# Optimization experiments

Hardware: AMD Instinct MI355X
Metric: run time of the kernel (lower is better)

The kernel has to match this reference:

```python
import jax, jax.numpy as jnp
import numpy as np

B = 1024      # jets per batch
P = 150       # TOTAL_PARTICLES per jet
N = B * P     # total nodes
DEG = 16      # avg degree
E = N * DEG
H = 256       # GNN_HIDDEN_DIM
K = 6         # GNN_K
NC = 10       # NUM_CLUSTERS
IN = 3


def setup_inputs() -> dict:
    key = jax.random.key(0)
    ks = jax.random.split(key, 16)
    x = jax.random.normal(ks[0], (N, IN), jnp.float32)
    # kNN-like within-jet edges: each node sends to DEG random nodes of its own jet
    src = jnp.repeat(jnp.arange(N, dtype=jnp.int32), DEG)
    tgt = (src // P) * P + jax.random.randint(ks[1], (E,), 0, P, dtype=jnp.int32)
    edge_index = jnp.stack([src, tgt])  # [2, E]
    batch = jnp.arange(N, dtype=jnp.int32) // P  # sorted graph ids, exactly P per graph
    inp = dict(x=x, edge_index=edge_index, batch=batch)
    dims = [(IN, H), (H, H), (H, H), (H, H)]
    for i, (di, do) in enumerate(dims):
        s = 1.0 / np.sqrt(di)
        inp[f"W{i+1}"] = jax.random.uniform(ks[2 + i], (K, di, do), jnp.float32, -s, s)
        inp[f"b{i+1}"] = jnp.zeros((do,), jnp.float32)
    for i in range(3):
        inp[f"g{i+1}"] = jnp.ones((H,), jnp.float32)
        inp[f"be{i+1}"] = jnp.zeros((H,), jnp.float32)
    inp["centers"] = jax.random.normal(ks[10], (NC, 2), jnp.float32) * 0.2
    inp["log_temp"] = jnp.float32(2.0)
    return inp


def _lap_weights(src, tgt, n):
    # PyG ChebConv norm with lambda_max=2, sym normalization, self-loops removed:
    # scaled Laplacian L_hat = -D^{-1/2} A D^{-1/2} (zero diagonal)
    w = (src != tgt).astype(jnp.float32)          # remove self-loops
    deg = jax.ops.segment_sum(w, src, num_segments=n)
    dis = jnp.where(deg > 0, 1.0 / jnp.sqrt(deg), 0.0)
    return -(dis[src] * w * dis[tgt])             # [E]


def _cheb(x, W, b, src, tgt, lw, n):
    # Chebyshev recurrence: T0=x, T1=Lx, Tk=2L T_{k-1} - T_{k-2}
    prop = lambda h: jax.ops.segment_sum(lw[:, None] * h[src], tgt, num_segments=n)
    Tx0 = x
    out = Tx0 @ W[0]
    Tx1 = prop(Tx0)
    out = out + Tx1 @ W[1]
    for k in range(2, W.shape[0]):
        Tx2 = 2.0 * prop(Tx1) - Tx0
        out = out + Tx2 @ W[k]
        Tx0, Tx1 = Tx1, Tx2
    return out + b


def _bn(h, g, b):
    # BatchNorm1d, training-mode batch statistics (biased var), eps=1e-5
    m = h.mean(0)
    v = h.var(0)
    return (h - m) * jax.lax.rsqrt(v + 1e-5) * g + b


def reference(x, edge_index, batch, W1, b1, W2, b2, W3, b3, W4, b4,
              g1, be1, g2, be2, g3, be3, centers, log_temp):
    n = x.shape[0]
    src, tgt = edge_index[0], edge_index[1]
    lw = _lap_weights(src, tgt, n)
    lrelu = lambda h: jax.nn.leaky_relu(h, 0.01)
    h = lrelu(_bn(_cheb(x, W1, b1, src, tgt, lw, n), g1, be1))
    h = lrelu(_bn(_cheb(h, W2, b2, src, tgt, lw, n), g2, be2))
    h = lrelu(_bn(_cheb(h, W3, b3, src, tgt, lw, n), g3, be3))
    h = _cheb(h, W4, b4, src, tgt, lw, n)
    h = h / jnp.maximum(jnp.linalg.norm(h, axis=1, keepdims=True), 1e-12)  # F.normalize
    # to_dense_batch: batch is sorted with exactly P nodes per graph -> pure reshape,
    # node_mask is all True
    dense_h = h.reshape(B, P, -1)          # [B, P, H]
    dense_c = x[:, :2].reshape(B, P, 2)    # (eta, phi)
    dist = ((dense_c[:, :, None, :] - centers) ** 2).sum(-1)   # [B, P, NC]
    T = jnp.exp(jnp.clip(log_temp, -2.0, 3.0))
    assignment = jax.nn.softmax(-T * dist, axis=-1)            # mask is all-true
    pooled = jnp.einsum('bnk,bnd->bkd', assignment, dense_h)   # [B, NC, H]
    pooled = pooled / (assignment.sum(1)[:, :, None] + 1e-8)
    return pooled.reshape(B, -1)  # [B, NC*H]
```

## Files before the change

### kernel.cpp

```cpp
#include <hip/hip_runtime.h>
#include <cstdio>

#define NODES 153600
#define PJ 150
#define NJETS 1024
#define DEG 16
#define NEDGE (NODES*DEG)
#define HD 256
#define NCL 10

#define LSTR 192
#define TNS  64

typedef unsigned short u16;
typedef _Float16 f16;
typedef f16 f16x8 __attribute__((ext_vector_type(8)));
typedef u16 u16x8 __attribute__((ext_vector_type(8)));
typedef u16 u16x4 __attribute__((ext_vector_type(4)));
typedef float f32x4 __attribute__((ext_vector_type(4)));

__device__ inline float h2f(u16 u) { union { u16 s; f16 h; } v; v.s = u; return (float)v.h; }
__device__ inline u16 f2h(float f) { union { u16 s; f16 h; } v; v.h = (f16)f; return v.s; }
__device__ inline int swz(int seg, int key) { return (seg & ~7) | ((seg & 7) ^ (key & 7)); }

__global__ void k_diag(float* out, float code) {
  if (blockIdx.x == 0 && threadIdx.x == 0) out[0] = code;
}


__global__ __launch_bounds__(256) void k_discounts(const int* __restrict__ tgt,
                                                   int* __restrict__ counts,
                                                   float* __restrict__ dis) {
  int i = blockIdx.x*256 + threadIdx.x;
  if (i < NEDGE) atomicAdd(&counts[tgt[i]], 1);
  if (i < NODES) {
    int cnt = 0;
#pragma unroll
    for (int j = 0; j < DEG; ++j) cnt += (tgt[i*DEG + j] != i) ? 1 : 0;
    dis[i] = (cnt > 0) ? rsqrtf((float)cnt) : 0.f;
  }
}

__global__ __launch_bounds__(256) void k_scan(const int* __restrict__ counts, int* __restrict__ rowptr, int* __restrict__ cursor) {
  int j = blockIdx.x*256 + threadIdx.x;
  if (j >= NJETS) return;
  int run = j*PJ*DEG;
  for (int l = 0; l < PJ; ++l) {
    int idx = j*PJ + l;
    int cnt = counts[idx];
    rowptr[idx] = run;
    cursor[idx] = run;
    run += cnt;
  }
  if (j == 0) rowptr[NODES] = NEDGE;
}

__global__ __launch_bounds__(256) void k_fill(const int* __restrict__ src_, const int* __restrict__ tgt_,
                                              const float* __restrict__ dis, int* __restrict__ cursor,
                                              unsigned char* __restrict__ ccol, float* __restrict__ cw) {
  int e = blockIdx.x*256 + threadIdx.x;
  if (e >= NEDGE) return;
  int s = src_[e], t = tgt_[e];
  int pos = atomicAdd(&cursor[t], 1);
  ccol[pos] = (unsigned char)(s % PJ);
  cw[pos] = (s != t) ? -(dis[s]*dis[t]) : 0.f;
}

__global__ __launch_bounds__(256) void k_prepLW(const int* __restrict__ rowptr,
                                                const unsigned char* __restrict__ ccol,
                                                const float* __restrict__ cw,
                                                u16* __restrict__ Lg,
                                                const float* __restrict__ Wa, const float* __restrict__ Wb,
                                                const float* __restrict__ Wc, u16* __restrict__ WT,
                                                float* __restrict__ s1, float* __restrict__ s2,
                                                float* __restrict__ rn) {
  int bid = blockIdx.x, tid = threadIdx.x;
  if (bid < NJETS) {
    int j = bid;
    u16* L = Lg + (size_t)j*160*160;
    if (tid < 160) {
      u16x8 z = {0,0,0,0,0,0,0,0};
      for (int seg = 0; seg < 20; ++seg) *(u16x8*)&L[tid*160 + seg*8] = z;
      if (tid < PJ) {
        int es = rowptr[j*PJ + tid], ee = rowptr[j*PJ + tid + 1];
        u16* row = L + tid*160;
        for (int e = es; e < ee; ++e) {
          int c = (int)ccol[e];
          row[c] = f2h(h2f(row[c]) + 2.f*cw[e]);
        }
      }
    }
  } else {
    int i = (bid - NJETS)*256 + tid;
    if (i < 3*256*1536) {
      int layer = i / (256*1536);
      int rem = i - layer*(256*1536);
      int cout = rem / 1536, k = rem - cout*1536;
      int term = k >> 8, cin = k & 255;
      const float* W = (layer == 0) ? Wa : (layer == 1) ? Wb : Wc;
      WT[i] = f2h(W[(size_t)term*65536 + cin*256 + cout]);
    }
    if (i < 2*HD) { s1[i] = 0.f; s2[i] = 0.f; }
    if (i < NODES) rn[i] = 0.f;
  }
}

__global__ __launch_bounds__(512) void k_cheb3(const float* __restrict__ x,
                                               const int* __restrict__ rowptr,
                                               const unsigned char* __restrict__ ccol,
                                               const float* __restrict__ cw,
                                               float* __restrict__ tall,
                                               float* __restrict__ s0) {
  __shared__ float Ta[450], Tb[450];
  __shared__ float cw_s[PJ*DEG];
  __shared__ u16  col_s[PJ*DEG];
  __shared__ int  rp_s[PJ+1];
  int j = blockIdx.x, tid = threadIdx.x;
  if (j == 0 && tid < 2*HD) s0[tid] = 0.f;
  int jb = j*PJ, e0 = jb*DEG;
  for (int i = tid; i < PJ*DEG; i += 512) { cw_s[i] = cw[e0+i]; col_s[i] = (u16)ccol[e0+i]; }
  for (int i = tid; i < PJ+1; i += 512) rp_s[i] = rowptr[jb+i] - e0;
  if (tid < 450) Ta[tid] = x[(size_t)jb*3 + tid];
  __syncthreads();
  int r = tid/3, c = tid - r*3;
  float* cur = Ta; float* oth = Tb;
  if (tid < 450) tall[(size_t)(jb+r)*18 + c] = cur[tid];
  for (int t = 1; t < 6; ++t) {
    if (tid < 450) {
      int es = rp_s[r], ee = rp_s[r+1];
      float acc = 0.f;
      for (int e = es; e < ee; ++e) acc += cw_s[e]*cur[(int)col_s[e]*3 + c];
      float v = (t == 1) ? acc : 2.f*acc - oth[tid];
      oth[tid] = v;
      tall[(size_t)(jb+r)*18 + t*3 + c] = v;
    }
    __syncthreads();
    float* tmp = cur; cur = oth; oth = tmp;
  }
}

__global__ __launch_bounds__(256) void k_gemm1(const float* __restrict__ tall, const float* __restrict__ W1,
                                               const float* __restrict__ b1, float* __restrict__ stats,
                                               u16* __restrict__ outc) {
  __shared__ float wl[18*256];
  __shared__ float tl[64*18];
  int c = threadIdx.x;
  for (int i = c; i < 18*256; i += 256) wl[i] = W1[i];
  int n0 = blockIdx.x*64;
  __syncthreads();
  for (int i = c; i < 64*18; i += 256) tl[i] = tall[(size_t)n0*18 + i];
  __syncthreads();
  float bc = b1[c];
  float s = 0.f, s2 = 0.f;
  for (int n = 0; n < 64; ++n) {
    float acc = 0.f;
#pragma unroll
    for (int i = 0; i < 18; ++i) acc += tl[n*18 + i] * wl[i*256 + c];
    outc[(size_t)(n0+n)*HD + c] = f2h(acc);
    float vb = acc + bc;
    s += vb; s2 += vb*vb;
  }
  atomicAdd(&stats[c], s);
  atomicAdd(&stats[HD + c], s2);
}

template<int OMODE>
__global__ __launch_bounds__(1024, 4) void k_cheb(const u16* __restrict__ IN,
                                                  const u16* __restrict__ WTu,
                                                  const u16* __restrict__ Lg,
                                                  const float* __restrict__ statsPrev,
                                                  const float* __restrict__ gP,
                                                  const float* __restrict__ beP,
                                                  const float* __restrict__ bP,
                                                  const float* __restrict__ bCur,
                                                  float* __restrict__ statsCur,
                                                  float* __restrict__ rn,
                                                  u16* __restrict__ OUTp) {
  __shared__ u16 Ls[160*LSTR];
  __shared__ u16 Tn[2][160*TNS];
  __shared__ u16 Tt[2][64*LSTR];
  __shared__ float bnA[HD], bnB[HD];
  int j = blockIdx.x, tid = threadIdx.x;
  int jb = j*PJ;
  int lane = tid & 63, wid = tid >> 6;
  int wm = wid >> 3, wn = wid & 7;
  int lr = lane & 15, lg = lane >> 4;
  int ph = wn >> 2, cs = wn & 3;
  int cown = cs*16 + lr;
  int key   = lr & 7;
  int segA0 = ((lg    ) ^ key) * 8;
  int segA1 = ((lg + 4) ^ key) * 8;
  int pOff[5] = { segA0, segA1, 64 + segA0, 64 + segA1, 128 + segA0 };
  int ep0 = ((cown >> 3) ^ ((lg & 1)*4 + 0)) * 8 + (cown & 7);
  int ep1 = ((cown >> 3) ^ ((lg & 1)*4 + 1)) * 8 + (cown & 7);
  int ep2 = ((cown >> 3) ^ ((lg & 1)*4 + 2)) * 8 + (cown & 7);
  int ep3 = ((cown >> 3) ^ ((lg & 1)*4 + 3)) * 8 + (cown & 7);
  int cownL = cown * LSTR;
  const f16* WT = (const f16*)WTu;
  const f16* wtb = WT + (size_t)(wn*32 + lr)*1536 + lg*8;

  if (tid < HD) {
    const float invN = 1.f/(float)NODES;
    float m = statsPrev[tid]*invN;
    float var = statsPrev[HD+tid]*invN - m*m;
    float A = rsqrtf(var + 1e-5f) * gP[tid];
    bnA[tid] = A;
    bnB[tid] = (bP[tid] - m)*A + beP[tid];
  }
  {
    const u16* src = Lg + (size_t)j*25600;
    for (int i = tid; i < 3200; i += 1024) {
      int row = i/20, seg = i - row*20;
      *(u16x8*)&Ls[row*LSTR + swz(seg,row)*8] = *(const u16x8*)&src[row*160 + seg*8];
    }
  }
  f32x4 acc[5][2];
#pragma unroll
  for (int a = 0; a < 5; ++a)
#pragma unroll
    for (int b = 0; b < 2; ++b) acc[a][b] = (f32x4)0.f;

  u16x4 tc0, tc1, tc2, tc3, tc4, tp0, tp1, tp2, tp3, tp4;

  for (int qp = 0; qp < 2; ++qp) {
    __syncthreads();
    for (int i = tid; i < 2560; i += 1024) {
      int h = (i >= 1280) ? 1 : 0;
      int rem = i - h*1280;
      int row = rem >> 3, seg = rem & 7;
      u16x8 o = {0,0,0,0,0,0,0,0};
      if (row < PJ) {
        int c0 = (qp*2+h)*64 + seg*8;
        u16x8 v = *(const u16x8*)&IN[(size_t)(jb+row)*HD + c0];
#pragma unroll
        for (int u = 0; u < 8; ++u) {
          float f = h2f(v[u])*bnA[c0+u] + bnB[c0+u];
          o[u] = f2h((f > 0.f) ? f : 0.01f*f);
        }
      }
      *(u16x8*)&Tn[h][row*TNS + (seg ^ (row & 7))*8] = o;
    }
    __syncthreads();
    for (int i = tid; i < 2560; i += 1024) {
      int h = (i >= 1280) ? 1 : 0;
      int rem = i - h*1280;
      int c = rem & 63, m = rem >> 6;
      u16x8 v;
#pragma unroll
      for (int u = 0; u < 8; ++u) {
        int r = m*8 + u;
        v[u] = Tn[h][r*TNS + ((c >> 3) ^ (r & 7))*8 + (c & 7)];
      }
      *(u16x8*)&Tt[h][c*LSTR + swz(m, c)*8] = v;
    }
#define TINIT(MF, TC, TP) { int r0 = wm*80 + MF*16 + lg*4; u16x4 t; \
    t[0] = Tn[ph][(r0+0)*TNS + ep0]; t[1] = Tn[ph][(r0+1)*TNS + ep1]; \
    t[2] = Tn[ph][(r0+2)*TNS + ep2]; t[3] = Tn[ph][(r0+3)*TNS + ep3]; \
    TC = t; TP = t; }
    TINIT(0, tc0, tp0) TINIT(1, tc1, tp1) TINIT(2, tc2, tp2) TINIT(3, tc3, tp3) TINIT(4, tc4, tp4)
#undef TINIT
    __syncthreads();
#pragma unroll 1
    for (int t = 0; t < 6; ++t) {
#pragma unroll
      for (int h = 0; h < 2; ++h) {
        int kbase = t*256 + (qp*2+h)*64;
#pragma unroll
        for (int ks = 0; ks < 64; ks += 32) {
          int segA = (ks == 0) ? segA0 : segA1;
          f16x8 a[5], bv[2];
#pragma unroll
          for (int nf = 0; nf < 2; ++nf)
            bv[nf] = *(const f16x8*)&wtb[nf*24576 + kbase + ks];
#pragma unroll
          for (int mf = 0; mf < 5; ++mf) {
            int row = wm*80 + mf*16 + lr;
            a[mf] = *(const f16x8*)&Tn[h][row*TNS + segA];
          }
#pragma unroll
          for (int nf = 0; nf < 2; ++nf)
#pragma unroll
            for (int mf = 0; mf < 5; ++mf)
              acc[mf][nf] = __builtin_amdgcn_mfma_f32_16x16x32_f16(a[mf], bv[nf], acc[mf][nf], 0, 0, 0);
        }
      }
      if (t < 5) {
        f32x4 pacc[5];
#pragma unroll
        for (int mf = 0; mf < 5; ++mf) pacc[mf] = (f32x4)0.f;
#pragma unroll
        for (int ks = 0; ks < 5; ++ks) {
          f16x8 b = *(const f16x8*)&Tt[ph][cownL + pOff[ks]];
#pragma unroll
          for (int mf = 0; mf < 5; ++mf) {
            int row = wm*80 + mf*16 + lr;
            f16x8 a = *(const f16x8*)&Ls[row*LSTR + pOff[ks]];
            pacc[mf] = __builtin_amdgcn_mfma_f32_16x16x32_f16(a, b, pacc[mf], 0, 0, 0);
          }
        }
        __syncthreads();
#define TEPI(MF, TC, TP) { int r0 = wm*80 + MF*16 + lg*4; u16x4 o; \
        { float v0_ = (t == 0) ? 0.5f*pacc[MF][0] : pacc[MF][0] - h2f(TP[0]); o[0] = f2h(v0_); } \
        { float v1_ = (t == 0) ? 0.5f*pacc[MF][1] : pacc[MF][1] - h2f(TP[1]); o[1] = f2h(v1_); } \
        { float v2_ = (t == 0) ? 0.5f*pacc[MF][2] : pacc[MF][2] - h2f(TP[2]); o[2] = f2h(v2_); } \
        { float v3_ = (t == 0) ? 0.5f*pacc[MF][3] : pacc[MF][3] - h2f(TP[3]); o[3] = f2h(v3_); } \
        Tn[ph][(r0+0)*TNS + ep0] = o[0]; Tn[ph][(r0+1)*TNS + ep1] = o[1]; \
        Tn[ph][(r0+2)*TNS + ep2] = o[2]; Tn[ph][(r0+3)*TNS + ep3] = o[3]; \
        int sgT = wm*10 + MF*2 + (lg >> 1); \
        int segT = (sgT & ~7) | ((sgT & 7) ^ key); \
        *(u16x4*)&Tt[ph][cownL + segT*8 + (lg & 1)*4] = o; \
        TP = TC; TC = o; }
        TEPI(0, tc0, tp0) TEPI(1, tc1, tp1) TEPI(2, tc2, tp2) TEPI(3, tc3, tp3) TEPI(4, tc4, tp4)
#undef TEPI
        __syncthreads();
      }
    }
  }
  if (OMODE == 0) {
#pragma unroll
    for (int nf = 0; nf < 2; ++nf) {
      int col = wn*32 + nf*16 + lr;
      float bc = bCur[col];
      float s = 0.f, s2 = 0.f;
#pragma unroll
      for (int mf = 0; mf < 5; ++mf) {
        int row = wm*80 + mf*16 + lg*4;
#pragma unroll
        for (int e = 0; e < 4; ++e) {
          int r = row + e;
          if (r < PJ) {
            float v = acc[mf][nf][e];
            OUTp[(size_t)(jb+r)*HD + col] = f2h(v);
            float vb = v + bc;
            s += vb; s2 += vb*vb;
          }
        }
      }
      s  += __shfl_xor(s, 16, 64);  s  += __shfl_xor(s, 32, 64);
      s2 += __shfl_xor(s2, 16, 64); s2 += __shfl_xor(s2, 32, 64);
      if (lg == 0) {
        atomicAdd(&statsCur[col], s);
        atomicAdd(&statsCur[HD + col], s2);
      }
    }
  } else {
    float bc[2];
#pragma unroll
    for (int nf = 0; nf < 2; ++nf) bc[nf] = bCur[wn*32 + nf*16 + lr];
#pragma unroll
    for (int mf = 0; mf < 5; ++mf) {
      int row = wm*80 + mf*16 + lg*4;
#pragma unroll
      for (int e = 0; e < 4; ++e) {
        int r = row + e;
        float srow = 0.f;
        if (r < PJ) {
#pragma unroll
          for (int nf = 0; nf < 2; ++nf) {
            int col = wn*32 + nf*16 + lr;
            float v = acc[mf][nf][e];
            OUTp[(size_t)(jb+r)*HD + col] = f2h(v);
            float vb = v + bc[nf];
            srow += vb*vb;
          }
        }
        srow += __shfl_xor(srow, 1, 64);
        srow += __shfl_xor(srow, 2, 64);
        srow += __shfl_xor(srow, 4, 64);
        srow += __shfl_xor(srow, 8, 64);
        if (lr == 0 && r < PJ) atomicAdd(&rn[jb + r], srow);
      }
    }
  }
}


__global__ __launch_bounds__(256) void k_pool(const u16* __restrict__ h, const float* __restrict__ rn,
                                              const float* __restrict__ bias, const float* __restrict__ x,
                                              const float* __restrict__ centers, const float* __restrict__ log_temp,
                                              float* __restrict__ out) {
  __shared__ float a_s[PJ][NCL];
  __shared__ float colsum[NCL];
  __shared__ float inv_s[PJ];
  int j = blockIdx.x;
  int tid = threadIdx.x;
  float T = expf(fminf(fmaxf(log_temp[0], -2.f), 3.f));
  if (tid < PJ) {
    int g = j*PJ + tid;
    inv_s[tid] = 1.f / fmaxf(sqrtf(rn[g]), 1e-12f);
    float eta = x[(size_t)g*3], phi = x[(size_t)g*3 + 1];
    float d[NCL];
    float dmin = 1e30f;
#pragma unroll
    for (int k = 0; k < NCL; ++k) {
      float dx = eta - centers[2*k], dy = phi - centers[2*k+1];
      d[k] = dx*dx + dy*dy;
      dmin = fminf(dmin, d[k]);
    }
    float s = 0.f, ek[NCL];
#pragma unroll
    for (int k = 0; k < NCL; ++k) { ek[k] = expf(-T*(d[k]-dmin)); s += ek[k]; }
    float invs = 1.f/s;
#pragma unroll
    for (int k = 0; k < NCL; ++k) a_s[tid][k] = ek[k]*invs;
  }
  __syncthreads();
  if (tid < NCL) {
    float s = 0.f;
    for (int n = 0; n < PJ; ++n) s += a_s[n][tid];
    colsum[tid] = s;
  }
  __syncthreads();
  int c = tid;
  float bc = bias[c];
  float acc[NCL] = {};
  for (int n = 0; n < PJ; ++n) {
    float hv = (h2f(h[(size_t)(j*PJ + n)*HD + c]) + bc) * inv_s[n];
#pragma unroll
    for (int k = 0; k < NCL; ++k) acc[k] += a_s[n][k]*hv;
  }
#pragma unroll
  for (int k = 0; k < NCL; ++k)
    out[(size_t)j*(NCL*HD) + k*HD + c] = acc[k] / (colsum[k] + 1e-8f);
}


extern "C" void kernel_launch(void* const* d_in, const int* in_sizes, int n_in,
                              void* d_out, int out_size, void* d_ws, size_t ws_size,
                              hipStream_t stream) {
  (void)in_sizes; (void)n_in; (void)out_size;
  const float* x   = (const float*)d_in[0];
  const int*   ei  = (const int*)d_in[1];
  const int*   srcA = ei;
  const int*   tgtA = ei + NEDGE;
  const float* W1  = (const float*)d_in[3];
  const float* b1  = (const float*)d_in[4];
  const float* W2  = (const float*)d_in[5];
  const float* b2  = (const float*)d_in[6];
  const float* W3  = (const float*)d_in[7];
  const float* b3  = (const float*)d_in[8];
  const float* W4  = (const float*)d_in[9];
  const float* b4  = (const float*)d_in[10];
  const float* g1  = (const float*)d_in[11];
  const float* be1 = (const float*)d_in[12];
  const float* g2  = (const float*)d_in[13];
  const float* be2 = (const float*)d_in[14];
  const float* g3  = (const float*)d_in[15];
  const float* be3 = (const float*)d_in[16];
  const float* centers  = (const float*)d_in[17];
  const float* log_temp = (const float*)d_in[18];
  float* out = (float*)d_out;

  auto rb = [](size_t b) { return (b + 255) & ~(size_t)255; };
  size_t need = 3*rb((size_t)NODES*HD*2)
              + 3*rb((size_t)NODES*4)
              + rb((size_t)(NODES+1)*4)
              + rb((size_t)NEDGE)
              + rb((size_t)NEDGE*4)
              + rb((size_t)3*2*HD*4)
              + rb((size_t)NODES*4);
  fprintf(stderr, "[kernel_launch] ws_size=%zu need=%zu\n", ws_size, need);
  if (d_ws == nullptr || ws_size < need) {
    float code = 1.0e6f + (float)(ws_size >> 20);
    k_diag<<<1, 1, 0, stream>>>(out, code);
    return;
  }

  char* wp = (char*)d_ws;
  auto alloc = [&](size_t b) -> void* {
    void* p = (void*)wp;
    wp += (b + 255) & ~(size_t)255;
    return p;
  };
  u16*   OUTA = (u16*)alloc((size_t)NODES*HD*2);
  u16*   OUTB = (u16*)alloc((size_t)NODES*HD*2);
  u16*   Y    = (u16*)alloc((size_t)NODES*HD*2);
  float* dis  = (float*)alloc((size_t)NODES*4);
  int*   counts = (int*)alloc((size_t)NODES*4);
  int*   cursor = (int*)alloc((size_t)NODES*4);
  int*   rowptr = (int*)alloc((size_t)(NODES+1)*4);
  unsigned char* ccol = (unsigned char*)alloc((size_t)NEDGE);
  float* cw     = (float*)alloc((size_t)NEDGE*4);
  float* stats  = (float*)alloc((size_t)3*2*HD*4);
  float* rn     = (float*)alloc((size_t)NODES*4);
  float* Tall = (float*)Y;
  u16*   Lg   = Y;
  u16*   Wcat = Y + (size_t)NJETS*160*160;
  float* s0 = stats, *s1 = stats + 512, *s2 = stats + 1024;

  hipMemsetAsync(counts, 0, (size_t)NODES*4, stream);
  k_discounts<<<(NEDGE+255)/256, 256, 0, stream>>>(tgtA, counts, dis);
  k_scan<<<(NJETS+255)/256, 256, 0, stream>>>(counts, rowptr, cursor);
  k_fill<<<(NEDGE+255)/256, 256, 0, stream>>>(srcA, tgtA, dis, cursor, ccol, cw);

  k_cheb3<<<NJETS, 512, 0, stream>>>(x, rowptr, ccol, cw, Tall, s0);
  k_gemm1<<<NODES/64, 256, 0, stream>>>(Tall, W1, b1, s0, OUTA);

  k_prepLW<<<NJETS + (3*256*1536+255)/256, 256, 0, stream>>>(rowptr, ccol, cw, Lg,
                                                             W2, W3, W4, Wcat, s1, s2, rn);

  k_cheb<0><<<NJETS, 1024, 0, stream>>>(OUTA, Wcat,            Lg, s0, g1, be1, b1, b2, s1, rn, OUTB);
  k_cheb<0><<<NJETS, 1024, 0, stream>>>(OUTB, Wcat + 393216,   Lg, s1, g2, be2, b2, b3, s2, rn, OUTA);
  k_cheb<1><<<NJETS, 1024, 0, stream>>>(OUTA, Wcat + 2*393216, Lg, s2, g3, be3, b3, b4, s2, rn, OUTB);

  k_pool<<<NJETS, 256, 0, stream>>>(OUTB, rn, b4, x, centers, log_temp, out);
}
```

Baseline: 1.351 ms.

## Fuse layer-1 Chebyshev with its GEMM and build dense Laplacian in-kernel

Merges k_cheb3 and k_gemm1 into one per-jet kernel so the Chebyshev terms stay in shared memory and are never written to and re-read from global memory. The dense per-jet Laplacian is no longer materialised in global memory by k_prepLW; each k_cheb block zeroes its shared tile and scatters the CSR edges into it directly. The edge scatter is repeated in each of the three layer kernels and runs serially per row inside the block, and padding rows are zeroed once instead of on every load. This removes about 50MB of global Laplacian traffic and one launch, and shrinks the workspace.

```diff
diff --git a/kernel.cpp b/kernel.cpp
--- a/kernel.cpp
+++ b/kernel.cpp
@@ -66,65 +66,47 @@
   cw[pos] = (s != t) ? -(dis[s]*dis[t]) : 0.f;
 }
 
-__global__ __launch_bounds__(256) void k_prepLW(const int* __restrict__ rowptr,
-                                                const unsigned char* __restrict__ ccol,
-                                                const float* __restrict__ cw,
-                                                u16* __restrict__ Lg,
-                                                const float* __restrict__ Wa, const float* __restrict__ Wb,
-                                                const float* __restrict__ Wc, u16* __restrict__ WT,
-                                                float* __restrict__ s1, float* __restrict__ s2,
-                                                float* __restrict__ rn) {
-  int bid = blockIdx.x, tid = threadIdx.x;
-  if (bid < NJETS) {
-    int j = bid;
-    u16* L = Lg + (size_t)j*160*160;
-    if (tid < 160) {
-      u16x8 z = {0,0,0,0,0,0,0,0};
-      for (int seg = 0; seg < 20; ++seg) *(u16x8*)&L[tid*160 + seg*8] = z;
-      if (tid < PJ) {
-        int es = rowptr[j*PJ + tid], ee = rowptr[j*PJ + tid + 1];
-        u16* row = L + tid*160;
-        for (int e = es; e < ee; ++e) {
-          int c = (int)ccol[e];
-          row[c] = f2h(h2f(row[c]) + 2.f*cw[e]);
-        }
-      }
-    }
-  } else {
-    int i = (bid - NJETS)*256 + tid;
-    if (i < 3*256*1536) {
-      int layer = i / (256*1536);
-      int rem = i - layer*(256*1536);
-      int cout = rem / 1536, k = rem - cout*1536;
-      int term = k >> 8, cin = k & 255;
-      const float* W = (layer == 0) ? Wa : (layer == 1) ? Wb : Wc;
-      WT[i] = f2h(W[(size_t)term*65536 + cin*256 + cout]);
-    }
-    if (i < 2*HD) { s1[i] = 0.f; s2[i] = 0.f; }
-    if (i < NODES) rn[i] = 0.f;
-  }
-}
-
-__global__ __launch_bounds__(512) void k_cheb3(const float* __restrict__ x,
-                                               const int* __restrict__ rowptr,
-                                               const unsigned char* __restrict__ ccol,
-                                               const float* __restrict__ cw,
-                                               float* __restrict__ tall,
-                                               float* __restrict__ s0) {
+__global__ __launch_bounds__(256) void k_prepW(const float* __restrict__ Wa, const float* __restrict__ Wb,
+                                               const float* __restrict__ Wc, u16* __restrict__ WT,
+                                               float* __restrict__ stats ,
+                                               float* __restrict__ rn) {
+  int i = blockIdx.x*256 + threadIdx.x;
+  if (i < 3*256*1536) {
+    int layer = i / (256*1536);
+    int rem = i - layer*(256*1536);
+    int cout = rem / 1536, k = rem - cout*1536;
+    int term = k >> 8, cin = k & 255;
+    const float* W = (layer == 0) ? Wa : (layer == 1) ? Wb : Wc;
+    WT[i] = f2h(W[(size_t)term*65536 + cin*256 + cout]);
+  }
+  if (i < 3*2*HD) stats[i] = 0.f;
+  if (i < NODES) rn[i] = 0.f;
+}
+
+__global__ __launch_bounds__(512) void k_l1(const float* __restrict__ x,
+                                            const int* __restrict__ rowptr,
+                                            const unsigned char* __restrict__ ccol,
+                                            const float* __restrict__ cw,
+                                            const float* __restrict__ W1,
+                                            const float* __restrict__ b1,
+                                            float* __restrict__ stats,
+                                            u16* __restrict__ outc) {
   __shared__ float Ta[450], Tb[450];
+  __shared__ float Tall_s[PJ*18];
+  __shared__ float wl[18*256];
   __shared__ float cw_s[PJ*DEG];
   __shared__ u16  col_s[PJ*DEG];
   __shared__ int  rp_s[PJ+1];
   int j = blockIdx.x, tid = threadIdx.x;
-  if (j == 0 && tid < 2*HD) s0[tid] = 0.f;
   int jb = j*PJ, e0 = jb*DEG;
+  for (int i = tid; i < 18*256; i += 512) wl[i] = W1[i];
   for (int i = tid; i < PJ*DEG; i += 512) { cw_s[i] = cw[e0+i]; col_s[i] = (u16)ccol[e0+i]; }
   for (int i = tid; i < PJ+1; i += 512) rp_s[i] = rowptr[jb+i] - e0;
   if (tid < 450) Ta[tid] = x[(size_t)jb*3 + tid];
   __syncthreads();
   int r = tid/3, c = tid - r*3;
   float* cur = Ta; float* oth = Tb;
-  if (tid < 450) tall[(size_t)(jb+r)*18 + c] = cur[tid];
+  if (tid < 450) Tall_s[r*18 + c] = cur[tid];
   for (int t = 1; t < 6; ++t) {
     if (tid < 450) {
       int es = rp_s[r], ee = rp_s[r+1];
@@ -132,42 +114,33 @@
       for (int e = es; e < ee; ++e) acc += cw_s[e]*cur[(int)col_s[e]*3 + c];
       float v = (t == 1) ? acc : 2.f*acc - oth[tid];
       oth[tid] = v;
-      tall[(size_t)(jb+r)*18 + t*3 + c] = v;
+      Tall_s[r*18 + t*3 + c] = v;
     }
     __syncthreads();
     float* tmp = cur; cur = oth; oth = tmp;
   }
-}
-
-__global__ __launch_bounds__(256) void k_gemm1(const float* __restrict__ tall, const float* __restrict__ W1,
-                                               const float* __restrict__ b1, float* __restrict__ stats,
-                                               u16* __restrict__ outc) {
-  __shared__ float wl[18*256];
-  __shared__ float tl[64*18];
-  int c = threadIdx.x;
-  for (int i = c; i < 18*256; i += 256) wl[i] = W1[i];
-  int n0 = blockIdx.x*64;
-  __syncthreads();
-  for (int i = c; i < 64*18; i += 256) tl[i] = tall[(size_t)n0*18 + i];
-  __syncthreads();
-  float bc = b1[c];
+  int cc = tid & 255, rhalf = tid >> 8;
+  float bc = b1[cc];
   float s = 0.f, s2 = 0.f;
-  for (int n = 0; n < 64; ++n) {
+  int r0 = rhalf*75;
+  for (int rr = r0; rr < r0 + 75; ++rr) {
     float acc = 0.f;
 #pragma unroll
-    for (int i = 0; i < 18; ++i) acc += tl[n*18 + i] * wl[i*256 + c];
-    outc[(size_t)(n0+n)*HD + c] = f2h(acc);
+    for (int i = 0; i < 18; ++i) acc += Tall_s[rr*18 + i] * wl[i*256 + cc];
+    outc[(size_t)(jb+rr)*HD + cc] = f2h(acc);
     float vb = acc + bc;
     s += vb; s2 += vb*vb;
   }
-  atomicAdd(&stats[c], s);
-  atomicAdd(&stats[HD + c], s2);
+  atomicAdd(&stats[cc], s);
+  atomicAdd(&stats[HD + cc], s2);
 }
 
 template<int OMODE>
 __global__ __launch_bounds__(1024, 4) void k_cheb(const u16* __restrict__ IN,
                                                   const u16* __restrict__ WTu,
-                                                  const u16* __restrict__ Lg,
+                                                  const int* __restrict__ rowptr,
+                                                  const unsigned char* __restrict__ ccol,
+                                                  const float* __restrict__ cw,
                                                   const float* __restrict__ statsPrev,
                                                   const float* __restrict__ gP,
                                                   const float* __restrict__ beP,
@@ -208,10 +181,22 @@
     bnB[tid] = (bP[tid] - m)*A + beP[tid];
   }
   {
-    const u16* src = Lg + (size_t)j*25600;
-    for (int i = tid; i < 3200; i += 1024) {
-      int row = i/20, seg = i - row*20;
-      *(u16x8*)&Ls[row*LSTR + swz(seg,row)*8] = *(const u16x8*)&src[row*160 + seg*8];
+    u16x8 z = {0,0,0,0,0,0,0,0};
+    for (int i = tid; i < 3840; i += 1024) *(u16x8*)&Ls[i*8] = z;
+    for (int i = tid; i < 160; i += 1024) {
+      int h = i >= 80 ? 1 : 0;
+      int rem = i - h*80;
+      int row = 150 + (rem >> 3), seg = rem & 7;
+      *(u16x8*)&Tn[h][row*TNS + seg*8] = z;
+    }
+  }
+  __syncthreads();
+  if (tid < PJ) {
+    int es = rowptr[jb + tid], ee = rowptr[jb + tid + 1];
+    for (int e = es; e < ee; ++e) {
+      int c = (int)ccol[e];
+      int a = tid*LSTR + swz(c >> 3, tid)*8 + (c & 7);
+      Ls[a] = f2h(h2f(Ls[a]) + 2.f*cw[e]);
     }
   }
   f32x4 acc[5][2];
@@ -224,19 +209,17 @@
 
   for (int qp = 0; qp < 2; ++qp) {
     __syncthreads();
-    for (int i = tid; i < 2560; i += 1024) {
-      int h = (i >= 1280) ? 1 : 0;
-      int rem = i - h*1280;
+    for (int i = tid; i < 2400; i += 1024) {
+      int h = (i >= 1200) ? 1 : 0;
+      int rem = i - h*1200;
       int row = rem >> 3, seg = rem & 7;
-      u16x8 o = {0,0,0,0,0,0,0,0};
-      if (row < PJ) {
-        int c0 = (qp*2+h)*64 + seg*8;
-        u16x8 v = *(const u16x8*)&IN[(size_t)(jb+row)*HD + c0];
-#pragma unroll
-        for (int u = 0; u < 8; ++u) {
-          float f = h2f(v[u])*bnA[c0+u] + bnB[c0+u];
-          o[u] = f2h((f > 0.f) ? f : 0.01f*f);
-        }
+      int c0 = (qp*2+h)*64 + seg*8;
+      u16x8 v = *(const u16x8*)&IN[(size_t)(jb+row)*HD + c0];
+      u16x8 o;
+#pragma unroll
+      for (int u = 0; u < 8; ++u) {
+        float f = h2f(v[u])*bnA[c0+u] + bnB[c0+u];
+        o[u] = f2h((f > 0.f) ? f : 0.01f*f);
       }
       *(u16x8*)&Tn[h][row*TNS + (seg ^ (row & 7))*8] = o;
     }
@@ -452,7 +435,8 @@
   float* out = (float*)d_out;
 
   auto rb = [](size_t b) { return (b + 255) & ~(size_t)255; };
-  size_t need = 3*rb((size_t)NODES*HD*2)
+  size_t need = 2*rb((size_t)NODES*HD*2)
+              + rb((size_t)3*256*1536*2)
               + 3*rb((size_t)NODES*4)
               + rb((size_t)(NODES+1)*4)
               + rb((size_t)NEDGE)
@@ -474,7 +458,7 @@
   };
   u16*   OUTA = (u16*)alloc((size_t)NODES*HD*2);
   u16*   OUTB = (u16*)alloc((size_t)NODES*HD*2);
-  u16*   Y    = (u16*)alloc((size_t)NODES*HD*2);
+  u16*   Wcat = (u16*)alloc((size_t)3*256*1536*2);
   float* dis  = (float*)alloc((size_t)NODES*4);
   int*   counts = (int*)alloc((size_t)NODES*4);
   int*   cursor = (int*)alloc((size_t)NODES*4);
@@ -483,9 +467,6 @@
   float* cw     = (float*)alloc((size_t)NEDGE*4);
   float* stats  = (float*)alloc((size_t)3*2*HD*4);
   float* rn     = (float*)alloc((size_t)NODES*4);
-  float* Tall = (float*)Y;
-  u16*   Lg   = Y;
-  u16*   Wcat = Y + (size_t)NJETS*160*160;
   float* s0 = stats, *s1 = stats + 512, *s2 = stats + 1024;
 
   hipMemsetAsync(counts, 0, (size_t)NODES*4, stream);
@@ -493,15 +474,13 @@
   k_scan<<<(NJETS+255)/256, 256, 0, stream>>>(counts, rowptr, cursor);
   k_fill<<<(NEDGE+255)/256, 256, 0, stream>>>(srcA, tgtA, dis, cursor, ccol, cw);
 
-  k_cheb3<<<NJETS, 512, 0, stream>>>(x, rowptr, ccol, cw, Tall, s0);
-  k_gemm1<<<NODES/64, 256, 0, stream>>>(Tall, W1, b1, s0, OUTA);
-
-  k_prepLW<<<NJETS + (3*256*1536+255)/256, 256, 0, stream>>>(rowptr, ccol, cw, Lg,
-                                                             W2, W3, W4, Wcat, s1, s2, rn);
-
-  k_cheb<0><<<NJETS, 1024, 0, stream>>>(OUTA, Wcat,            Lg, s0, g1, be1, b1, b2, s1, rn, OUTB);
-  k_cheb<0><<<NJETS, 1024, 0, stream>>>(OUTB, Wcat + 393216,   Lg, s1, g2, be2, b2, b3, s2, rn, OUTA);
-  k_cheb<1><<<NJETS, 1024, 0, stream>>>(OUTA, Wcat + 2*393216, Lg, s2, g3, be3, b3, b4, s2, rn, OUTB);
+  k_prepW<<<(3*256*1536+255)/256, 256, 0, stream>>>(W2, W3, W4, Wcat, stats, rn);
+
+  k_l1<<<NJETS, 512, 0, stream>>>(x, rowptr, ccol, cw, W1, b1, s0, OUTA);
+
+  k_cheb<0><<<NJETS, 1024, 0, stream>>>(OUTA, Wcat,            rowptr, ccol, cw, s0, g1, be1, b1, b2, s1, rn, OUTB);
+  k_cheb<0><<<NJETS, 1024, 0, stream>>>(OUTB, Wcat + 393216,   rowptr, ccol, cw, s1, g2, be2, b2, b3, s2, rn, OUTA);
+  k_cheb<1><<<NJETS, 1024, 0, stream>>>(OUTA, Wcat + 2*393216, rowptr, ccol, cw, s2, g3, be3, b3, b4, s2, rn, OUTB);
 
   k_pool<<<NJETS, 256, 0, stream>>>(OUTB, rn, b4, x, centers, log_temp, out);
 }
```

Measured after the change: 1.273 ms. 5.8% less time.
